# Kernel optimization log

Hardware: AMD Instinct MI355X
Metric: run time of the kernel (lower is better)

The kernel has to match this reference:

```python
import jax, jax.numpy as jnp
import numpy as np

B, S, D, H, L, FF = 1, 2048, 512, 8, 4, 2048
DH = D // H


def _sincos(n, d):
    theta = 1.0 / (10000.0 ** (np.arange(0, d, 2, dtype=np.float64) / d))
    ang = np.arange(n, dtype=np.float64)[:, None] * theta[None, :]
    sin = np.repeat(np.sin(ang), 2, axis=-1).astype(np.float32)
    cos = np.repeat(np.cos(ang), 2, axis=-1).astype(np.float32)
    return jnp.asarray(sin), jnp.asarray(cos)  # [n, d]


def _rot(x):
    # rotate pairs: (x1, x2) -> (-x2, x1), interleaved
    x1, x2 = x[..., 0::2], x[..., 1::2]
    return jnp.stack([-x2, x1], axis=-1).reshape(x.shape)


def _theta_shift(x, sin, cos):
    return x * cos + _rot(x) * sin


def _decay_mask(n, h):
    # RetNet per-head decay gammas: 1 - exp(linspace(log(1/32), log(1/512), h))
    gammas = 1.0 - np.exp(np.linspace(np.log(1.0 / 32.0), np.log(1.0 / 512.0), h))
    dist = np.arange(n)[:, None] - np.arange(n)[None, :]
    m = np.where(dist >= 0, gammas[:, None, None] ** np.maximum(dist, 0), 0.0)
    return jnp.asarray(m, dtype=jnp.float32)  # [h, n, n]


def _ln(x, w, b, eps=1e-5):
    mu = x.mean(-1, keepdims=True)
    var = ((x - mu) ** 2).mean(-1, keepdims=True)
    return (x - mu) * jax.lax.rsqrt(var + eps) * w + b


def setup_inputs() -> dict:
    key = jax.random.key(0)
    ks = jax.random.split(key, 12)
    sc = 0.02
    nrm = lambda k, shp: jax.random.normal(k, shp, jnp.float32) * sc
    return {
        "x": jax.random.normal(ks[0], (B, S, D), jnp.float32),
        "pos_emb": nrm(ks[1], (5000, D)),
        "Wq": nrm(ks[2], (L, D, D)), "bq": jnp.zeros((L, D), jnp.float32),
        "Wk": nrm(ks[3], (L, D, D)), "bk": jnp.zeros((L, D), jnp.float32),
        "Wv": nrm(ks[4], (L, D, D)), "bv": jnp.zeros((L, D), jnp.float32),
        "Wg": nrm(ks[5], (L, D, D)), "bg": jnp.zeros((L, D), jnp.float32),
        "Wo": nrm(ks[6], (L, D, D)), "bo": jnp.zeros((L, D), jnp.float32),
        "ln1w": jnp.ones((L, D), jnp.float32), "ln1b": jnp.zeros((L, D), jnp.float32),
        "ln2w": jnp.ones((L, D), jnp.float32), "ln2b": jnp.zeros((L, D), jnp.float32),
        "W1": nrm(ks[7], (L, D, FF)), "b1": jnp.zeros((L, FF), jnp.float32),
        "W2": nrm(ks[8], (L, FF, D)), "b2": jnp.zeros((L, D), jnp.float32),
        "Wout": nrm(ks[9], (D, 1)), "bout": jnp.zeros((1,), jnp.float32),
    }


def reference(x, pos_emb, Wq, bq, Wk, bk, Wv, bv, Wg, bg, Wo, bo,
              ln1w, ln1b, ln2w, ln2b, W1, b1, W2, b2, Wout, bout):
    b, s, d = x.shape
    # faithful to source: pos_emb[:x.shape[0]] (requires B==1 to broadcast)
    x = x + pos_emb[: x.shape[0]]
    sin, cos = _sincos(s, DH)
    dmask = _decay_mask(s, H)  # [h, s, s]
    inv_scale = 1.0 / jnp.sqrt(jnp.float32(DH))

    def heads(t):  # [b,s,d] -> [b,h,s,dh]
        return t.reshape(b, s, H, DH).transpose(0, 2, 1, 3)

    for l in range(L):
        # --- multi-scale retention block (pre-LN) ---
        y = _ln(x, ln1w[l], ln1b[l])
        q = heads(y @ Wq[l] + bq[l])
        k = heads(y @ Wk[l] + bk[l])
        v = heads(y @ Wv[l] + bv[l])
        q = _theta_shift(q, sin, cos) * inv_scale
        k = _theta_shift(k, sin, cos)
        sim = jnp.einsum("bhnd,bhmd->bhnm", q, k) * dmask  # decay-masked QK^T
        ret = jnp.einsum("bhnm,bhmd->bhnd", sim, v)
        # per-head group norm (no affine)
        mu = ret.mean(-1, keepdims=True)
        var = ((ret - mu) ** 2).mean(-1, keepdims=True)
        ret = (ret - mu) * jax.lax.rsqrt(var + 1e-6)
        ret = ret.transpose(0, 2, 1, 3).reshape(b, s, d)
        g = jax.nn.silu(y @ Wg[l] + bg[l])
        x = x + (g * ret) @ Wo[l] + bo[l]
        # --- FFN block (pre-LN, swish) ---
        z = _ln(x, ln2w[l], ln2b[l])
        x = x + jax.nn.silu(z @ W1[l] + b1[l]) @ W2[l] + b2[l]

    return jax.nn.sigmoid(x @ Wout + bout)  # [b, s, 1]
```

## Files before the change

### kernel.cpp

```cpp
#include <hip/hip_runtime.h>
#include <math.h>
#include <stdint.h>

#define SEQ 2048
#define DMODEL 512
#define NH 8
#define DHEAD 64
#define NL 4
#define DFF 2048

typedef __attribute__((ext_vector_type(8))) short short8;
typedef __attribute__((ext_vector_type(4))) float f32x4;

__device__ __forceinline__ short f2bf(float f) {
  unsigned u = __float_as_uint(f);
  u += 0x7fffu + ((u >> 16) & 1u);
  return (short)(u >> 16);
}
__device__ __forceinline__ float silu_f(float x) { return x / (1.f + __expf(-x)); }

__device__ __forceinline__ void cp16(const void* g, void* l) {
  __builtin_amdgcn_global_load_lds(
      (const __attribute__((address_space(1))) unsigned*)(unsigned long long)(uintptr_t)g,
      (__attribute__((address_space(3))) unsigned*)(unsigned)(uintptr_t)l, 16, 0, 0);
}

struct TP { const float* src; short* dst; int rows, cols, base; };
struct TPs { TP t[7]; };
__global__ __launch_bounds__(256) void k_prep(TPs ts) {
  int bid = blockIdx.x;
  int di = 6;
  while (di > 0 && bid < ts.t[di].base) --di;
  TP d = ts.t[di];
  int local = bid - d.base;
  int tx = d.cols >> 5, ty = d.rows >> 5;
  int tpz = tx * ty;
  int z = local / tpz, rem = local - z * tpz;
  int bx = (rem % tx) * 32, by = (rem / tx) * 32;
  const float* src = d.src + (size_t)z * d.rows * d.cols;
  short* dst = d.dst + (size_t)z * d.rows * d.cols;
  __shared__ float tile[32][33];
  int txi = threadIdx.x & 31, tyi = threadIdx.x >> 5;
#pragma unroll
  for (int k = 0; k < 4; ++k)
    tile[tyi + k * 8][txi] = src[(size_t)(by + tyi + k * 8) * d.cols + bx + txi];
  __syncthreads();
#pragma unroll
  for (int k = 0; k < 4; ++k)
    dst[(size_t)(bx + tyi + k * 8) * d.rows + by + txi] = f2bf(tile[txi][tyi + k * 8]);
}

__global__ void k_init(const float* __restrict__ xi, const float* __restrict__ pos, float* __restrict__ xo,
                       float* __restrict__ sn, float* __restrict__ cs) {
  if (blockIdx.x < 1024) {
    int i = blockIdx.x * 256 + threadIdx.x;
    float4 a = ((const float4*)xi)[i];
    float4 p = ((const float4*)pos)[i & 127];
    a.x += p.x; a.y += p.y; a.z += p.z; a.w += p.w;
    ((float4*)xo)[i] = a;
  } else {
    int g = (blockIdx.x - 1024) * 256 + threadIdx.x;
    int s = g >> 5, p = g & 31;
    double inv = pow(10000.0, -(double)p / 32.0);
    double a = (double)s * inv;
    float sv = (float)sin(a), cv = (float)cos(a);
    sn[s * DHEAD + 2 * p] = sv; sn[s * DHEAD + 2 * p + 1] = sv;
    cs[s * DHEAD + 2 * p] = cv; cs[s * DHEAD + 2 * p + 1] = cv;
  }
}

__global__ __launch_bounds__(256) void k_ln(const float* __restrict__ x, const float* __restrict__ w,
                                            const float* __restrict__ b, short* __restrict__ o, float eps) {
  int wid = threadIdx.x >> 6, lane = threadIdx.x & 63;
  int row = blockIdx.x * 4 + wid;
  const float* xr = x + (size_t)row * DMODEL;
  float4 v0 = *(const float4*)(xr + lane * 8);
  float4 v1 = *(const float4*)(xr + lane * 8 + 4);
  float sm = v0.x + v0.y + v0.z + v0.w + v1.x + v1.y + v1.z + v1.w;
  float sq = v0.x * v0.x + v0.y * v0.y + v0.z * v0.z + v0.w * v0.w +
             v1.x * v1.x + v1.y * v1.y + v1.z * v1.z + v1.w * v1.w;
#pragma unroll
  for (int m = 1; m < 64; m <<= 1) { sm += __shfl_xor(sm, m); sq += __shfl_xor(sq, m); }
  float mu = sm * (1.f / 512.f);
  float rstd = rsqrtf(sq * (1.f / 512.f) - mu * mu + eps);
  const float* wr = w + lane * 8; const float* br = b + lane * 8;
  float vals[8] = {v0.x, v0.y, v0.z, v0.w, v1.x, v1.y, v1.z, v1.w};
  short t[8] __attribute__((aligned(16)));
#pragma unroll
  for (int i = 0; i < 8; ++i) t[i] = f2bf((vals[i] - mu) * rstd * wr[i] + br[i]);
  *(int4*)(o + (size_t)row * DMODEL + lane * 8) = *(int4*)t;
}

struct GB { const short* Bt; const float* bias; void* out; int mode; };
struct GP {
  const short* A;
  const float* sn; const float* cs;
  GB b[4];
  int M, N, K, kspl;
};

template <int BNT>
__global__ __launch_bounds__(256) void k_gemm(GP ga) {
  constexpr int NB = BNT / 32;
  constexpr int BRND = BNT / 32;
  const int z = blockIdx.z;
  GB gb; int k0, klen;
  if (ga.kspl > 0) { gb = ga.b[0]; k0 = z * ga.kspl; klen = ga.kspl; }
  else { gb = ga.b[z]; k0 = 0; klen = ga.K; }
  const int K = ga.K, N = ga.N, M = ga.M;
  const int n0 = blockIdx.x * BNT, m0 = blockIdx.y * 64;
  const int tid = threadIdx.x;
  const int w = tid >> 6, lane = tid & 63, l16 = lane & 15, quad = lane >> 4;
  const int wm = (w & 1) * 32, wn = (w >> 1) * (BNT / 2);
  const int nIter = klen >> 6;

  __shared__ __align__(16) short As[2][4096];
  __shared__ __align__(16) short Bs[2][BNT * 64];

  const short* Ab = ga.A + (size_t)m0 * K + k0;
  const short* Bb = gb.Bt + (size_t)n0 * K + k0;
  const int rsub = lane >> 3, cch = (lane & 7) ^ rsub;

  auto stage = [&](int buf, int it) {
#pragma unroll
    for (int c = 0; c < 2; ++c) {
      int seg = w + 4 * c;
      cp16(Ab + (size_t)(seg * 8 + rsub) * K + (it << 6) + cch * 8, &As[buf][seg * 512]);
    }
#pragma unroll
    for (int c = 0; c < BRND; ++c) {
      int seg = w + 4 * c;
      cp16(Bb + (size_t)(seg * 8 + rsub) * K + (it << 6) + cch * 8, &Bs[buf][seg * 512]);
    }
  };

  f32x4 acc[2][NB];
#pragma unroll
  for (int a = 0; a < 2; ++a)
#pragma unroll
    for (int b = 0; b < NB; ++b) acc[a][b] = {0.f, 0.f, 0.f, 0.f};

  stage(0, 0);
  for (int it = 0; it < nIter; ++it) {
    __syncthreads();
    if (it + 1 < nIter) stage((it + 1) & 1, it + 1);
    const short* as = As[it & 1];
    const short* bs = Bs[it & 1];
#pragma unroll
    for (int kki = 0; kki < 2; ++kki) {
      int ch = ((quad + 4 * kki) ^ (l16 & 7)) * 8;
      short8 af[2], bfv[NB];
#pragma unroll
      for (int a = 0; a < 2; ++a) af[a] = *(const short8*)&as[(wm + a * 16 + l16) * 64 + ch];
#pragma unroll
      for (int b = 0; b < NB; ++b) bfv[b] = *(const short8*)&bs[(wn + b * 16 + l16) * 64 + ch];
#pragma unroll
      for (int a = 0; a < 2; ++a)
#pragma unroll
        for (int b = 0; b < NB; ++b)
          acc[a][b] = __builtin_amdgcn_mfma_f32_16x16x32_bf16(af[a], bfv[b], acc[a][b], 0, 0, 0);
    }
  }

  const int mode = gb.mode;
#pragma unroll
  for (int a = 0; a < 2; ++a) {
#pragma unroll
    for (int b = 0; b < NB; ++b) {
      int row0 = m0 + wm + a * 16 + quad * 4;
      int col = n0 + wn + b * 16 + l16;
      float bi = (mode == 2 && k0 > 0) ? 0.f : gb.bias[col];
      float vals[4];
#pragma unroll
      for (int r = 0; r < 4; ++r) vals[r] = acc[a][b][r] + bi;
      if (mode == 5 || mode == 6) {
        float sc = (mode == 5) ? 0.125f : 1.f;
        int d = col & 63;
#pragma unroll
        for (int r = 0; r < 4; ++r) {
          int s = row0 + r;
          float vv = vals[r];
          float p = __shfl_xor(vv, 1);
          float rot = (col & 1) ? p : -p;
          float o = (vv * ga.cs[s * 64 + d] + rot * ga.sn[s * 64 + d]) * sc;
          ((short*)gb.out)[(size_t)s * DMODEL + col] = f2bf(o);
        }
      } else if (mode == 4) {
        short t4[4] __attribute__((aligned(8)));
#pragma unroll
        for (int r = 0; r < 4; ++r) t4[r] = f2bf(vals[r]);
        *(uint2*)&((short*)gb.out)[(size_t)col * M + row0] = *(const uint2*)t4;
      } else if (mode == 0) {
#pragma unroll
        for (int r = 0; r < 4; ++r) ((float*)gb.out)[(size_t)(row0 + r) * N + col] = vals[r];
      } else if (mode == 1) {
#pragma unroll
        for (int r = 0; r < 4; ++r) ((short*)gb.out)[(size_t)(row0 + r) * N + col] = f2bf(silu_f(vals[r]));
      } else {
#pragma unroll
        for (int r = 0; r < 4; ++r) atomicAdd(&((float*)gb.out)[(size_t)(row0 + r) * N + col], vals[r]);
      }
    }
  }
}

__global__ __launch_bounds__(256) void k_attn(const short* __restrict__ qb, const short* __restrict__ kb,
                                              const short* __restrict__ vtb, float* __restrict__ r0,
                                              float* __restrict__ r1) {
  int x = blockIdx.x, hd = blockIdx.y, jc = blockIdx.z;
  int ib = jc ? (31 - x) : x;
  int t = threadIdx.x;
  int w = t >> 6, lane = t & 63, l16 = lane & 15, quad = lane >> 4;
  __shared__ __align__(16) short smem[4 * 64 * 72];
  short* qs = smem;
  short* kt = smem + 4608;
  short* vt = smem + 9216;
  short* p  = smem + 13824;

  double stepd = (log(1.0 / 512.0) - log(1.0 / 32.0)) / 7.0;
  double gam = 1.0 - exp(log(1.0 / 32.0) + hd * stepd);
  float l2g = (float)(log(gam) * 1.4426950408889634);

  for (int c = t; c < 512; c += 256) {
    int r = c >> 3, d8 = (c & 7) * 8;
    *(short8*)&qs[r * 72 + d8] = *(const short8*)&qb[(size_t)(ib * 64 + r) * DMODEL + hd * DHEAD + d8];
  }
  f32x4 oacc[4];
#pragma unroll
  for (int b = 0; b < 4; ++b) oacc[b] = {0.f, 0.f, 0.f, 0.f};

  for (int jb = jc; jb <= ib; jb += 2) {
    __syncthreads();
    for (int c = t; c < 512; c += 256) {
      int r = c >> 3, d8 = (c & 7) * 8;
      *(short8*)&kt[r * 72 + d8] = *(const short8*)&kb[(size_t)(jb * 64 + r) * DMODEL + hd * DHEAD + d8];
      *(short8*)&vt[r * 72 + d8] = *(const short8*)&vtb[(size_t)(hd * DHEAD + r) * SEQ + jb * 64 + d8];
    }
    __syncthreads();
    f32x4 sacc[4];
#pragma unroll
    for (int b = 0; b < 4; ++b) sacc[b] = {0.f, 0.f, 0.f, 0.f};
#pragma unroll
    for (int kk = 0; kk < 64; kk += 32) {
      short8 af = *(const short8*)&qs[(w * 16 + l16) * 72 + kk + quad * 8];
#pragma unroll
      for (int b = 0; b < 4; ++b) {
        short8 bf_ = *(const short8*)&kt[(b * 16 + l16) * 72 + kk + quad * 8];
        sacc[b] = __builtin_amdgcn_mfma_f32_16x16x32_bf16(af, bf_, sacc[b], 0, 0, 0);
      }
    }
    int dtile = (ib - jb) * 64;
#pragma unroll
    for (int b = 0; b < 4; ++b) {
#pragma unroll
      for (int r = 0; r < 4; ++r) {
        int iloc = w * 16 + quad * 4 + r;
        int jloc = b * 16 + l16;
        int df = dtile + iloc - jloc;
        float dec = (df < 0) ? 0.f : exp2f(l2g * (float)df);
        p[iloc * 72 + jloc] = f2bf(sacc[b][r] * dec);
      }
    }
    __syncthreads();
#pragma unroll
    for (int kk = 0; kk < 64; kk += 32) {
      short8 af = *(const short8*)&vt[(w * 16 + l16) * 72 + kk + quad * 8];
#pragma unroll
      for (int b = 0; b < 4; ++b) {
        short8 bf_ = *(const short8*)&p[(b * 16 + l16) * 72 + kk + quad * 8];
        oacc[b] = __builtin_amdgcn_mfma_f32_16x16x32_bf16(af, bf_, oacc[b], 0, 0, 0);
      }
    }
  }
  __syncthreads();
  float* obuf = (float*)smem;
#pragma unroll
  for (int b = 0; b < 4; ++b) {
#pragma unroll
    for (int r = 0; r < 4; ++r) {
      int d = w * 16 + quad * 4 + r;
      int i = b * 16 + l16;
      obuf[i * 68 + d] = oacc[b][r];
    }
  }
  __syncthreads();
  float* rp = jc ? r1 : r0;
  for (int c = t; c < 1024; c += 256) {
    int r = c >> 4, d4 = (c & 15) * 4;
    *(float4*)&rp[(size_t)(ib * 64 + r) * DMODEL + hd * DHEAD + d4] = *(const float4*)&obuf[r * 68 + d4];
  }
}

__global__ __launch_bounds__(256) void k_retgate(const float* __restrict__ r0, const float* __restrict__ r1,
                                                 const float* __restrict__ g, short* __restrict__ o) {
  int wid = threadIdx.x >> 6, lane = threadIdx.x & 63;
  int row = blockIdx.x * 4 + wid;
  int s = row >> 3, hd = row & 7;
  size_t base = (size_t)s * DMODEL + hd * DHEAD + lane;
  float v = r0[base] + r1[base];
  float sm = v, sq = v * v;
#pragma unroll
  for (int m = 1; m < 64; m <<= 1) { sm += __shfl_xor(sm, m); sq += __shfl_xor(sq, m); }
  float mu = sm * (1.f / 64.f);
  float var = sq * (1.f / 64.f) - mu * mu;
  float rn = (v - mu) * rsqrtf(var + 1e-6f);
  o[base] = f2bf(silu_f(g[base]) * rn);
}

__global__ __launch_bounds__(256) void k_final(const float* __restrict__ x, const float* __restrict__ w,
                                               const float* __restrict__ bo, float* __restrict__ o) {
  int wid = threadIdx.x >> 6, lane = threadIdx.x & 63;
  int row = blockIdx.x * 4 + wid;
  const float* xr = x + (size_t)row * DMODEL;
  float4 a0 = *(const float4*)(xr + lane * 8), a1 = *(const float4*)(xr + lane * 8 + 4);
  float4 w0 = *(const float4*)(w + lane * 8), w1 = *(const float4*)(w + lane * 8 + 4);
  float sm = a0.x * w0.x + a0.y * w0.y + a0.z * w0.z + a0.w * w0.w +
             a1.x * w1.x + a1.y * w1.y + a1.z * w1.z + a1.w * w1.w;
#pragma unroll
  for (int m = 1; m < 64; m <<= 1) sm += __shfl_xor(sm, m);
  if (lane == 0) o[row] = 1.f / (1.f + __expf(-(sm + bo[0])));
}

extern "C" void kernel_launch(void* const* d_in, const int* in_sizes, int n_in,
                              void* d_out, int out_size, void* d_ws, size_t ws_size,
                              hipStream_t stream) {
  const float* x_in = (const float*)d_in[0];
  const float* pos = (const float*)d_in[1];
  const float* Wq = (const float*)d_in[2];  const float* bq = (const float*)d_in[3];
  const float* Wk = (const float*)d_in[4];  const float* bk = (const float*)d_in[5];
  const float* Wv = (const float*)d_in[6];  const float* bv = (const float*)d_in[7];
  const float* Wg = (const float*)d_in[8];  const float* bg = (const float*)d_in[9];
  const float* Wo = (const float*)d_in[10]; const float* bo = (const float*)d_in[11];
  const float* ln1w = (const float*)d_in[12]; const float* ln1b = (const float*)d_in[13];
  const float* ln2w = (const float*)d_in[14]; const float* ln2b = (const float*)d_in[15];
  const float* W1 = (const float*)d_in[16]; const float* b1 = (const float*)d_in[17];
  const float* W2 = (const float*)d_in[18]; const float* b2 = (const float*)d_in[19];
  const float* Wout = (const float*)d_in[20]; const float* bout = (const float*)d_in[21];
  float* out = (float*)d_out;

  char* ws = (char*)d_ws;
  size_t off = 0;
  auto alloc = [&](size_t bytes) -> void* {
    void* p = ws + off;
    off += (bytes + 255) & ~(size_t)255;
    return p;
  };
  const size_t DD = (size_t)DMODEL * DMODEL;
  short* wqt = (short*)alloc((size_t)NL * DD * 2);
  short* wkt = (short*)alloc((size_t)NL * DD * 2);
  short* wvt = (short*)alloc((size_t)NL * DD * 2);
  short* wgt = (short*)alloc((size_t)NL * DD * 2);
  short* wot = (short*)alloc((size_t)NL * DD * 2);
  short* w1t = (short*)alloc((size_t)NL * DMODEL * DFF * 2);
  short* w2t = (short*)alloc((size_t)NL * DMODEL * DFF * 2);
  float* xb = (float*)alloc((size_t)SEQ * DMODEL * 4);
  short* ybf = (short*)alloc((size_t)SEQ * DMODEL * 2);
  float* graw = (float*)alloc((size_t)SEQ * DMODEL * 4);
  short* qb = (short*)alloc((size_t)SEQ * DMODEL * 2);
  short* kb = (short*)alloc((size_t)SEQ * DMODEL * 2);
  short* vtb = (short*)alloc((size_t)SEQ * DMODEL * 2);
  float* ret0 = (float*)alloc((size_t)SEQ * DMODEL * 4);
  float* ret1 = (float*)alloc((size_t)SEQ * DMODEL * 4);
  short* grb = (short*)alloc((size_t)SEQ * DMODEL * 2);
  short* zbf = (short*)alloc((size_t)SEQ * DMODEL * 2);
  short* hbf = (short*)alloc((size_t)SEQ * DFF * 2);
  float* sint = (float*)alloc((size_t)SEQ * DHEAD * 4);
  float* cost = (float*)alloc((size_t)SEQ * DHEAD * 4);

  TPs tp;
  tp.t[0] = TP{Wq, wqt, DMODEL, DMODEL, 0};
  tp.t[1] = TP{Wk, wkt, DMODEL, DMODEL, 1024};
  tp.t[2] = TP{Wv, wvt, DMODEL, DMODEL, 2048};
  tp.t[3] = TP{Wg, wgt, DMODEL, DMODEL, 3072};
  tp.t[4] = TP{Wo, wot, DMODEL, DMODEL, 4096};
  tp.t[5] = TP{W1, w1t, DMODEL, DFF, 5120};
  tp.t[6] = TP{W2, w2t, DFF, DMODEL, 9216};
  k_prep<<<13312, 256, 0, stream>>>(tp);
  k_init<<<1280, 256, 0, stream>>>(x_in, pos, xb, sint, cost);

  for (int l = 0; l < NL; ++l) {
    k_ln<<<SEQ / 4, 256, 0, stream>>>(xb, ln1w + l * DMODEL, ln1b + l * DMODEL, ybf, 1e-5f);

    GP gq{};
    gq.A = ybf; gq.sn = sint; gq.cs = cost;
    gq.b[0] = GB{wqt + l * DD, bq + l * DMODEL, qb, 5};
    gq.b[1] = GB{wkt + l * DD, bk + l * DMODEL, kb, 6};
    gq.b[2] = GB{wvt + l * DD, bv + l * DMODEL, vtb, 4};
    gq.b[3] = GB{wgt + l * DD, bg + l * DMODEL, graw, 0};
    gq.M = SEQ; gq.N = DMODEL; gq.K = DMODEL; gq.kspl = 0;
    k_gemm<128><<<dim3(DMODEL / 128, SEQ / 64, 4), 256, 0, stream>>>(gq);

    k_attn<<<dim3(32, NH, 2), 256, 0, stream>>>(qb, kb, vtb, ret0, ret1);
    k_retgate<<<SEQ * NH / 4, 256, 0, stream>>>(ret0, ret1, graw, grb);

    GP gw{};
    gw.A = grb;
    gw.b[0] = GB{wot + l * DD, bo + l * DMODEL, xb, 2};
    gw.M = SEQ; gw.N = DMODEL; gw.K = DMODEL; gw.kspl = 256;
    k_gemm<64><<<dim3(DMODEL / 64, SEQ / 64, 2), 256, 0, stream>>>(gw);

    k_ln<<<SEQ / 4, 256, 0, stream>>>(xb, ln2w + l * DMODEL, ln2b + l * DMODEL, zbf, 1e-5f);

    GP g1{};
    g1.A = zbf;
    g1.b[0] = GB{w1t + (size_t)l * DMODEL * DFF, b1 + l * DFF, hbf, 1};
    g1.M = SEQ; g1.N = DFF; g1.K = DMODEL; g1.kspl = 0;
    k_gemm<128><<<dim3(DFF / 128, SEQ / 64, 1), 256, 0, stream>>>(g1);

    GP g2{};
    g2.A = hbf;
    g2.b[0] = GB{w2t + (size_t)l * DMODEL * DFF, b2 + l * DMODEL, xb, 2};
    g2.M = SEQ; g2.N = DMODEL; g2.K = DFF; g2.kspl = 512;
    k_gemm<64><<<dim3(DMODEL / 64, SEQ / 64, 4), 256, 0, stream>>>(g2);
  }
  k_final<<<SEQ / 4, 256, 0, stream>>>(xb, Wout, bout, out);
}
```

Baseline: 548.2 us.

## Replace split-K atomics with partial buffers reduced inside layernorm

```diff
diff --git a/kernel.cpp b/kernel.cpp
--- a/kernel.cpp
+++ b/kernel.cpp
@@ -69,13 +69,25 @@
   }
 }
 
-__global__ __launch_bounds__(256) void k_ln(const float* __restrict__ x, const float* __restrict__ w,
-                                            const float* __restrict__ b, short* __restrict__ o, float eps) {
+__global__ __launch_bounds__(256) void k_ln(const float* __restrict__ x, const float* __restrict__ parts, int np,
+                                            const float* __restrict__ w, const float* __restrict__ b,
+                                            short* __restrict__ o, float eps, float* __restrict__ xout) {
   int wid = threadIdx.x >> 6, lane = threadIdx.x & 63;
   int row = blockIdx.x * 4 + wid;
-  const float* xr = x + (size_t)row * DMODEL;
-  float4 v0 = *(const float4*)(xr + lane * 8);
-  float4 v1 = *(const float4*)(xr + lane * 8 + 4);
+  size_t base = (size_t)row * DMODEL + lane * 8;
+  float4 v0 = *(const float4*)(x + base);
+  float4 v1 = *(const float4*)(x + base + 4);
+  for (int p = 0; p < np; ++p) {
+    const float* pp = parts + (size_t)p * SEQ * DMODEL;
+    float4 a0 = *(const float4*)(pp + base);
+    float4 a1 = *(const float4*)(pp + base + 4);
+    v0.x += a0.x; v0.y += a0.y; v0.z += a0.z; v0.w += a0.w;
+    v1.x += a1.x; v1.y += a1.y; v1.z += a1.z; v1.w += a1.w;
+  }
+  if (xout) {
+    *(float4*)(xout + base) = v0;
+    *(float4*)(xout + base + 4) = v1;
+  }
   float sm = v0.x + v0.y + v0.z + v0.w + v1.x + v1.y + v1.z + v1.w;
   float sq = v0.x * v0.x + v0.y * v0.y + v0.z * v0.z + v0.w * v0.w +
              v1.x * v1.x + v1.y * v1.y + v1.z * v1.z + v1.w * v1.w;
@@ -169,7 +181,7 @@
     for (int b = 0; b < NB; ++b) {
       int row0 = m0 + wm + a * 16 + quad * 4;
       int col = n0 + wn + b * 16 + l16;
-      float bi = (mode == 2 && k0 > 0) ? 0.f : gb.bias[col];
+      float bi = (mode == 2 && z > 0) ? 0.f : gb.bias[col];
       float vals[4];
 #pragma unroll
       for (int r = 0; r < 4; ++r) vals[r] = acc[a][b][r] + bi;
@@ -197,8 +209,9 @@
 #pragma unroll
         for (int r = 0; r < 4; ++r) ((short*)gb.out)[(size_t)(row0 + r) * N + col] = f2bf(silu_f(vals[r]));
       } else {
-#pragma unroll
-        for (int r = 0; r < 4; ++r) atomicAdd(&((float*)gb.out)[(size_t)(row0 + r) * N + col], vals[r]);
+        float* po = (float*)gb.out + (size_t)z * M * N;
+#pragma unroll
+        for (int r = 0; r < 4; ++r) po[(size_t)(row0 + r) * N + col] = vals[r];
       }
     }
   }
@@ -307,12 +320,20 @@
   o[base] = f2bf(silu_f(g[base]) * rn);
 }
 
-__global__ __launch_bounds__(256) void k_final(const float* __restrict__ x, const float* __restrict__ w,
-                                               const float* __restrict__ bo, float* __restrict__ o) {
+__global__ __launch_bounds__(256) void k_final(const float* __restrict__ x, const float* __restrict__ parts, int np,
+                                               const float* __restrict__ w, const float* __restrict__ bo,
+                                               float* __restrict__ o) {
   int wid = threadIdx.x >> 6, lane = threadIdx.x & 63;
   int row = blockIdx.x * 4 + wid;
-  const float* xr = x + (size_t)row * DMODEL;
-  float4 a0 = *(const float4*)(xr + lane * 8), a1 = *(const float4*)(xr + lane * 8 + 4);
+  size_t base = (size_t)row * DMODEL + lane * 8;
+  float4 a0 = *(const float4*)(x + base), a1 = *(const float4*)(x + base + 4);
+  for (int p = 0; p < np; ++p) {
+    const float* pp = parts + (size_t)p * SEQ * DMODEL;
+    float4 b0 = *(const float4*)(pp + base);
+    float4 b1 = *(const float4*)(pp + base + 4);
+    a0.x += b0.x; a0.y += b0.y; a0.z += b0.z; a0.w += b0.w;
+    a1.x += b1.x; a1.y += b1.y; a1.z += b1.z; a1.w += b1.w;
+  }
   float4 w0 = *(const float4*)(w + lane * 8), w1 = *(const float4*)(w + lane * 8 + 4);
   float sm = a0.x * w0.x + a0.y * w0.y + a0.z * w0.z + a0.w * w0.w +
              a1.x * w1.x + a1.y * w1.y + a1.z * w1.z + a1.w * w1.w;
@@ -346,6 +367,7 @@
     return p;
   };
   const size_t DD = (size_t)DMODEL * DMODEL;
+  const size_t SD = (size_t)SEQ * DMODEL;
   short* wqt = (short*)alloc((size_t)NL * DD * 2);
   short* wkt = (short*)alloc((size_t)NL * DD * 2);
   short* wvt = (short*)alloc((size_t)NL * DD * 2);
@@ -353,19 +375,21 @@
   short* wot = (short*)alloc((size_t)NL * DD * 2);
   short* w1t = (short*)alloc((size_t)NL * DMODEL * DFF * 2);
   short* w2t = (short*)alloc((size_t)NL * DMODEL * DFF * 2);
-  float* xb = (float*)alloc((size_t)SEQ * DMODEL * 4);
-  short* ybf = (short*)alloc((size_t)SEQ * DMODEL * 2);
-  float* graw = (float*)alloc((size_t)SEQ * DMODEL * 4);
-  short* qb = (short*)alloc((size_t)SEQ * DMODEL * 2);
-  short* kb = (short*)alloc((size_t)SEQ * DMODEL * 2);
-  short* vtb = (short*)alloc((size_t)SEQ * DMODEL * 2);
-  float* ret0 = (float*)alloc((size_t)SEQ * DMODEL * 4);
-  float* ret1 = (float*)alloc((size_t)SEQ * DMODEL * 4);
-  short* grb = (short*)alloc((size_t)SEQ * DMODEL * 2);
-  short* zbf = (short*)alloc((size_t)SEQ * DMODEL * 2);
+  float* xb = (float*)alloc(SD * 4);
+  short* ybf = (short*)alloc(SD * 2);
+  float* graw = (float*)alloc(SD * 4);
+  short* qb = (short*)alloc(SD * 2);
+  short* kb = (short*)alloc(SD * 2);
+  short* vtb = (short*)alloc(SD * 2);
+  float* ret0 = (float*)alloc(SD * 4);
+  float* ret1 = (float*)alloc(SD * 4);
+  short* grb = (short*)alloc(SD * 2);
+  short* zbf = (short*)alloc(SD * 2);
   short* hbf = (short*)alloc((size_t)SEQ * DFF * 2);
   float* sint = (float*)alloc((size_t)SEQ * DHEAD * 4);
   float* cost = (float*)alloc((size_t)SEQ * DHEAD * 4);
+  float* wpart = (float*)alloc(2 * SD * 4);
+  float* fpart = (float*)alloc(4 * SD * 4);
 
   TPs tp;
   tp.t[0] = TP{Wq, wqt, DMODEL, DMODEL, 0};
@@ -379,7 +403,9 @@
   k_init<<<1280, 256, 0, stream>>>(x_in, pos, xb, sint, cost);
 
   for (int l = 0; l < NL; ++l) {
-    k_ln<<<SEQ / 4, 256, 0, stream>>>(xb, ln1w + l * DMODEL, ln1b + l * DMODEL, ybf, 1e-5f);
+    k_ln<<<SEQ / 4, 256, 0, stream>>>(xb, fpart, l == 0 ? 0 : 4,
+                                      ln1w + l * DMODEL, ln1b + l * DMODEL, ybf, 1e-5f,
+                                      l == 0 ? nullptr : xb);
 
     GP gq{};
     gq.A = ybf; gq.sn = sint; gq.cs = cost;
@@ -388,30 +414,31 @@
     gq.b[2] = GB{wvt + l * DD, bv + l * DMODEL, vtb, 4};
     gq.b[3] = GB{wgt + l * DD, bg + l * DMODEL, graw, 0};
     gq.M = SEQ; gq.N = DMODEL; gq.K = DMODEL; gq.kspl = 0;
-    k_gemm<128><<<dim3(DMODEL / 128, SEQ / 64, 4), 256, 0, stream>>>(gq);
+    k_gemm<64><<<dim3(DMODEL / 64, SEQ / 64, 4), 256, 0, stream>>>(gq);
 
     k_attn<<<dim3(32, NH, 2), 256, 0, stream>>>(qb, kb, vtb, ret0, ret1);
     k_retgate<<<SEQ * NH / 4, 256, 0, stream>>>(ret0, ret1, graw, grb);
 
     GP gw{};
     gw.A = grb;
-    gw.b[0] = GB{wot + l * DD, bo + l * DMODEL, xb, 2};
+    gw.b[0] = GB{wot + l * DD, bo + l * DMODEL, wpart, 2};
     gw.M = SEQ; gw.N = DMODEL; gw.K = DMODEL; gw.kspl = 256;
     k_gemm<64><<<dim3(DMODEL / 64, SEQ / 64, 2), 256, 0, stream>>>(gw);
 
-    k_ln<<<SEQ / 4, 256, 0, stream>>>(xb, ln2w + l * DMODEL, ln2b + l * DMODEL, zbf, 1e-5f);
+    k_ln<<<SEQ / 4, 256, 0, stream>>>(xb, wpart, 2,
+                                      ln2w + l * DMODEL, ln2b + l * DMODEL, zbf, 1e-5f, xb);
 
     GP g1{};
     g1.A = zbf;
     g1.b[0] = GB{w1t + (size_t)l * DMODEL * DFF, b1 + l * DFF, hbf, 1};
     g1.M = SEQ; g1.N = DFF; g1.K = DMODEL; g1.kspl = 0;
-    k_gemm<128><<<dim3(DFF / 128, SEQ / 64, 1), 256, 0, stream>>>(g1);
+    k_gemm<64><<<dim3(DFF / 64, SEQ / 64, 1), 256, 0, stream>>>(g1);
 
     GP g2{};
     g2.A = hbf;
-    g2.b[0] = GB{w2t + (size_t)l * DMODEL * DFF, b2 + l * DMODEL, xb, 2};
+    g2.b[0] = GB{w2t + (size_t)l * DMODEL * DFF, b2 + l * DMODEL, fpart, 2};
     g2.M = SEQ; g2.N = DMODEL; g2.K = DFF; g2.kspl = 512;
     k_gemm<64><<<dim3(DMODEL / 64, SEQ / 64, 4), 256, 0, stream>>>(g2);
   }
-  k_final<<<SEQ / 4, 256, 0, stream>>>(xb, Wout, bout, out);
-}
+  k_final<<<SEQ / 4, 256, 0, stream>>>(xb, fpart, 4, Wout, bout, out);
+}
```

After: 521.0 us. -5.0%, faster.
